# Kernel tuning notes

Measured on AMD Instinct MI355X. Metric: run time of the kernel, lower is better.

Reference implementation:

```python
import jax, jax.numpy as jnp
import numpy as np

NUM_CLASSES = 80
S = 7            # grid_size
NB = 2           # num_boxes per cell
LAMBDA_COORD = 5.0
LAMBDA_NOOBJ = 0.5
N_BOX = 20       # padded boxes per image


def setup_inputs() -> dict:
    key = jax.random.key(0)
    k1, k2, k3, k4 = jax.random.split(key, 4)
    B = 4096
    predictions = jax.random.uniform(k1, (B, S, S, NB, 5 + NUM_CLASSES), dtype=jnp.float32)
    # build valid normalized xyxy boxes: centers in [0.1,0.9], half-sizes in [0.01,0.085]
    centers = jax.random.uniform(k2, (B, N_BOX, 2), dtype=jnp.float32) * 0.8 + 0.1
    half = jax.random.uniform(k3, (B, N_BOX, 2), dtype=jnp.float32) * 0.075 + 0.01
    targets_boxes = jnp.concatenate([centers - half, centers + half], axis=-1)
    targets_labels = jax.random.randint(k4, (B, N_BOX), 0, NUM_CLASSES)
    return {"predictions": predictions, "targets_boxes": targets_boxes, "targets_labels": targets_labels}


def encode_targets(boxes, labels):
    # boxes: [B,N,4] xyxy normalized; labels: [B,N] int
    B, N, _ = boxes.shape
    x = (boxes[..., 0] + boxes[..., 2]) * 0.5
    y = (boxes[..., 1] + boxes[..., 3]) * 0.5
    w = boxes[..., 2] - boxes[..., 0]
    h = boxes[..., 3] - boxes[..., 1]
    j = jnp.clip(jnp.floor(x * S).astype(jnp.int32), 0, S - 1)
    i = jnp.clip(jnp.floor(y * S).astype(jnp.int32), 0, S - 1)
    x_cell = x * S - j
    y_cell = y * S - i
    onehot = jax.nn.one_hot(labels, NUM_CLASSES, dtype=boxes.dtype)
    feats = jnp.concatenate([x_cell[..., None], y_cell[..., None], w[..., None], h[..., None],
                             jnp.ones_like(x_cell)[..., None], onehot], axis=-1)  # [B,N,5+C]
    bidx = jnp.arange(B, dtype=jnp.int32)[:, None]
    flat = ((bidx * S + i) * S + j).ravel()                       # [B*N] cell ids
    order = jnp.broadcast_to(jnp.arange(N, dtype=jnp.int32), (B, N)).ravel()
    winner = jnp.full((B * S * S,), N, dtype=jnp.int32).at[flat].min(order)
    cell_b = jnp.arange(B * S * S, dtype=jnp.int32) // (S * S)
    sel = jnp.minimum(winner, N - 1)
    grid = feats[cell_b, sel]
    grid = jnp.where((winner < N)[:, None], grid, jnp.zeros_like(grid))
    return grid.reshape(B, S, S, 5 + NUM_CLASSES)


def iou_xywh(a, b):
    ax1 = a[..., 0] - a[..., 2] * 0.5; ay1 = a[..., 1] - a[..., 3] * 0.5
    ax2 = a[..., 0] + a[..., 2] * 0.5; ay2 = a[..., 1] + a[..., 3] * 0.5
    bx1 = b[..., 0] - b[..., 2] * 0.5; by1 = b[..., 1] - b[..., 3] * 0.5
    bx2 = b[..., 0] + b[..., 2] * 0.5; by2 = b[..., 1] + b[..., 3] * 0.5
    iw = jnp.clip(jnp.minimum(ax2, bx2) - jnp.maximum(ax1, bx1), 0.0)
    ih = jnp.clip(jnp.minimum(ay2, by2) - jnp.maximum(ay1, by1), 0.0)
    inter = iw * ih
    union = (ax2 - ax1) * (ay2 - ay1) + (bx2 - bx1) * (by2 - by1) - inter
    return inter / (union + 1e-6)


def yolo_loss(predictions, targets_boxes, targets_labels):
    B = predictions.shape[0]
    tg = encode_targets(targets_boxes, targets_labels)   # [B,S,S,5+C]
    txy, twh = tg[..., :2], tg[..., 2:4]
    tconf, tcls = tg[..., 4:5], tg[..., 5:]
    obj = (tconf[..., 0] > 0).astype(predictions.dtype)   # [B,S,S]
    # responsible box = argmax IoU per cell, masked by obj
    pred_boxes = predictions[..., 0:4]                     # [B,S,S,NB,4]
    tgt_boxes = jnp.concatenate([txy, twh], axis=-1)[:, :, :, None, :]
    ious = iou_xywh(pred_boxes, jnp.broadcast_to(tgt_boxes, pred_boxes.shape))  # [B,S,S,NB]
    best = jnp.argmax(ious, axis=-1)
    resp = jax.nn.one_hot(best, NB, dtype=predictions.dtype) * obj[..., None]   # [B,S,S,NB]
    pxy = predictions[..., 0:2]; pwh = predictions[..., 2:4]
    pconf = predictions[..., 4:5]; pcls = predictions[..., 5:]
    om = obj[..., None, None]        # [B,S,S,1,1]
    rm = resp[..., None]             # [B,S,S,NB,1]
    loss_xy = LAMBDA_COORD * jnp.sum(om * rm * (pxy - txy[:, :, :, None, :]) ** 2) / B
    loss_wh = LAMBDA_COORD * jnp.sum(om * rm * (jnp.sqrt(jnp.clip(pwh, 1e-6)) - jnp.sqrt(jnp.clip(twh[:, :, :, None, :], 1e-6))) ** 2) / B
    loss_conf_obj = jnp.sum(om * rm * (pconf - tconf[:, :, :, None, :]) ** 2) / B
    loss_conf_noobj = LAMBDA_NOOBJ * jnp.sum((1.0 - obj)[..., None, None] * pconf ** 2) / B
    pred_cls_resp = jnp.sum(pcls * rm, axis=3)             # [B,S,S,C]
    loss_cls = jnp.sum(obj[..., None] * (pred_cls_resp - tcls) ** 2) / B
    return loss_xy + loss_wh + loss_conf_obj + loss_conf_noobj + loss_cls


def reference(predictions, targets_boxes, targets_labels):
    return yolo_loss(predictions, targets_boxes, targets_labels)
```

## Files before the change

kernel.cpp:

```cpp
#include <hip/hip_runtime.h>

#define S 7
#define NB 2
#define NC 80
#define NBOX 20
#define CELLS 49
#define CH 85
#define PAIR 170
#define PER_B 8330
#define NIMG 4096
#define NCELL_TOT (NIMG*CELLS)
#define N4TOT (NIMG*PER_B/4)
#define PREP_IMGS 4
#define PREP_BLOCKS (NIMG/PREP_IMGS)
#define STREAM_BLOCKS 2048
#define TSTRIDE (STREAM_BLOCKS*256)
#define L_COORD 5.0f
#define L_NOOBJ 0.5f

__device__ __forceinline__ void block_reduce_store(float acc, float* dst)
{
    __shared__ float s_wsum[4];
    int tid = threadIdx.x;
    #pragma unroll
    for (int off = 32; off > 0; off >>= 1) acc += __shfl_down(acc, off, 64);
    int lane = tid & 63, wv = tid >> 6;
    if (lane == 0) s_wsum[wv] = acc;
    __syncthreads();
    if (tid == 0) *dst = s_wsum[0] + s_wsum[1] + s_wsum[2] + s_wsum[3];
}

__global__ __launch_bounds__(256) void prep_kernel(
    const float* __restrict__ pred,
    const float* __restrict__ boxes,
    const int*   __restrict__ labels,
    float4*      __restrict__ wt4,
    float*       __restrict__ partial)
{
    __shared__ int   s_winner[PREP_IMGS * CELLS];
    __shared__ float s_cx[PREP_IMGS * NBOX], s_cy[PREP_IMGS * NBOX];
    __shared__ float s_bw[PREP_IMGS * NBOX], s_bh[PREP_IMGS * NBOX];
    __shared__ int   s_lab[PREP_IMGS * NBOX];

    const int b0  = blockIdx.x * PREP_IMGS;
    const int tid = threadIdx.x;

    if (tid < PREP_IMGS * CELLS) s_winner[tid] = NBOX;
    __syncthreads();

    if (tid < PREP_IMGS * NBOX) {
        int img = tid / NBOX, bxi = tid - img * NBOX;
        const float* bx = boxes + ((size_t)(b0 + img) * NBOX + bxi) * 4;
        float x1 = bx[0], y1 = bx[1], x2 = bx[2], y2 = bx[3];
        float x = (x1 + x2) * 0.5f, y = (y1 + y2) * 0.5f;
        s_cx[tid] = x; s_cy[tid] = y;
        s_bw[tid] = x2 - x1; s_bh[tid] = y2 - y1;
        s_lab[tid] = labels[(size_t)(b0 + img) * NBOX + bxi];
        int j = (int)floorf(x * (float)S); j = min(max(j, 0), S - 1);
        int i = (int)floorf(y * (float)S); i = min(max(i, 0), S - 1);
        atomicMin(&s_winner[img * CELLS + i * S + j], bxi);
    }
    __syncthreads();

    float acc = 0.0f;
    if (tid < PREP_IMGS * CELLS) {
        int img  = tid / CELLS;
        int cell = tid - img * CELLS;
        int w    = s_winner[tid];
        float4 wq;
        if (w < NBOX) {
            int i = cell / S, j = cell - (cell / S) * S;
            int bi = img * NBOX + w;
            float x = s_cx[bi], y = s_cy[bi];
            float tx = x * (float)S - (float)j;
            float ty = y * (float)S - (float)i;
            float tw = s_bw[bi], th = s_bh[bi];

            const float* p = pred + ((size_t)(b0 + img) * CELLS + cell) * PAIR;
            float bx1 = tx - tw * 0.5f, by1 = ty - th * 0.5f;
            float bx2 = tx + tw * 0.5f, by2 = ty + th * 0.5f;
            float barea = (bx2 - bx1) * (by2 - by1);
            float iou[2], px[2], py[2], pw[2], ph[2];
            #pragma unroll
            for (int nb = 0; nb < NB; nb++) {
                px[nb] = p[nb * CH + 0]; py[nb] = p[nb * CH + 1];
                pw[nb] = p[nb * CH + 2]; ph[nb] = p[nb * CH + 3];
                float ax1 = px[nb] - pw[nb] * 0.5f, ay1 = py[nb] - ph[nb] * 0.5f;
                float ax2 = px[nb] + pw[nb] * 0.5f, ay2 = py[nb] + ph[nb] * 0.5f;
                float iw = fmaxf(fminf(ax2, bx2) - fmaxf(ax1, bx1), 0.0f);
                float ih = fmaxf(fminf(ay2, by2) - fmaxf(ay1, by1), 0.0f);
                float inter = iw * ih;
                float uni = (ax2 - ax1) * (ay2 - ay1) + barea - inter;
                iou[nb] = inter / (uni + 1e-6f);
            }
            int resp = (iou[1] > iou[0]) ? 1 : 0;
            wq = (resp == 0) ? make_float4(1.f, 1.f, 0.f, 0.f)
                             : make_float4(0.f, 0.f, 1.f, 1.f);

            float pc = p[resp * CH + 4];
            float pl = p[resp * CH + 5 + s_lab[bi]];
            float dx = px[resp] - tx, dy = py[resp] - ty;
            float dw = sqrtf(fmaxf(pw[resp], 1e-6f)) - sqrtf(fmaxf(tw, 1e-6f));
            float dh = sqrtf(fmaxf(ph[resp], 1e-6f)) - sqrtf(fmaxf(th, 1e-6f));
            acc = L_COORD * (dx * dx + dy * dy + dw * dw + dh * dh)
                + (1.0f - 2.0f * pc)
                + (1.0f - 2.0f * pl);
        } else {
            wq = make_float4(L_NOOBJ, 0.f, L_NOOBJ, 0.f);
        }
        wt4[(size_t)(b0 + img) * CELLS + cell] = wq;
    }
    __syncthreads();
    block_reduce_store(acc, &partial[blockIdx.x]);
}

__device__ __forceinline__ float elem1(float p, int r, float4 w)
{
    int nb = (r >= CH) ? 1 : 0;
    int rr = r - nb * CH;
    float wconf = nb ? w.z : w.x;
    float wcls  = nb ? w.w : w.y;
    float m = (rr >= 5) ? wcls : ((rr == 4) ? wconf : 0.0f);
    return m * p * p;
}

__device__ __forceinline__ float elem4(float4 v, int e,
                                       const float4* __restrict__ wt4)
{
    unsigned ff = 4u * (unsigned)e;
    unsigned c0 = ff / (unsigned)PAIR;
    int r0 = (int)(ff - c0 * (unsigned)PAIR);
    float4 w0 = wt4[c0];
    float4 w1 = w0;
    bool wrap = (r0 == PAIR - 2);
    if (wrap) w1 = wt4[c0 + 1];
    int r2 = wrap ? 0 : r0 + 2;
    float a;
    a  = elem1(v.x, r0,     w0);
    a += elem1(v.y, r0 + 1, w0);
    a += elem1(v.z, r2,     w1);
    a += elem1(v.w, r2 + 1, w1);
    return a;
}

__global__ __launch_bounds__(256) void stream_kernel(
    const float4* __restrict__ p4,
    const float4* __restrict__ wt4,
    float*        __restrict__ partial)
{
    const int tid = threadIdx.x;
    const int gid = blockIdx.x * 256 + tid;

    float acc = 0.0f;
    int e = gid;
    #pragma unroll 8
    for (int k = 0; k < 16; ++k) {
        acc += elem4(p4[e], e, wt4);
        e += TSTRIDE;
    }
    if (e < N4TOT) acc += elem4(p4[e], e, wt4);

    block_reduce_store(acc, &partial[blockIdx.x]);
}

__global__ __launch_bounds__(256) void reduce_kernel(
    const float* __restrict__ partial, int n,
    float* __restrict__ out, float inv_B)
{
    const int tid = threadIdx.x;
    float acc = 0.0f;
    for (int i = tid; i < n; i += 256) acc += partial[i];
    __shared__ float s_wsum[4];
    #pragma unroll
    for (int off = 32; off > 0; off >>= 1) acc += __shfl_down(acc, off, 64);
    int lane = tid & 63, wv = tid >> 6;
    if (lane == 0) s_wsum[wv] = acc;
    __syncthreads();
    if (tid == 0) out[0] = (s_wsum[0] + s_wsum[1] + s_wsum[2] + s_wsum[3]) * inv_B;
}

extern "C" void kernel_launch(void* const* d_in, const int* in_sizes, int n_in,
                              void* d_out, int out_size, void* d_ws, size_t ws_size,
                              hipStream_t stream) {
    const float* pred   = (const float*)d_in[0];
    const float* boxes  = (const float*)d_in[1];
    const int*   labels = (const int*)d_in[2];

    float4* wt4          = (float4*)d_ws;
    float*  prep_part    = (float*)d_ws + (size_t)NCELL_TOT * 4;
    float*  stream_part  = prep_part + PREP_BLOCKS;

    prep_kernel<<<PREP_BLOCKS, 256, 0, stream>>>(pred, boxes, labels, wt4, prep_part);
    stream_kernel<<<STREAM_BLOCKS, 256, 0, stream>>>((const float4*)pred, wt4, stream_part);
    reduce_kernel<<<1, 256, 0, stream>>>(prep_part, PREP_BLOCKS + STREAM_BLOCKS,
                                         (float*)d_out, 1.0f / (float)NIMG);
}
```

Measured before the change: 203.3 us.

## Fuse target prep and prediction streaming into one per-image-pair kernel

Merges the prep and stream kernels so each block handles two images. It builds the per-cell weight table in shared memory and then streams that pair's predictions against it. This removes the global weight-table write and read-back and one kernel launch, and reads box coordinates as float4. The cost is 2048 blocks doing a serial prep phase before streaming, with reads that are contiguous per block rather than grid-strided, plus the cold per-cell prediction loads now on the critical path.

```diff
diff --git a/kernel.cpp b/kernel.cpp
--- a/kernel.cpp
+++ b/kernel.cpp
@@ -9,12 +9,10 @@
 #define PAIR 170
 #define PER_B 8330
 #define NIMG 4096
-#define NCELL_TOT (NIMG*CELLS)
-#define N4TOT (NIMG*PER_B/4)
-#define PREP_IMGS 4
-#define PREP_BLOCKS (NIMG/PREP_IMGS)
-#define STREAM_BLOCKS 2048
-#define TSTRIDE (STREAM_BLOCKS*256)
+#define IMGS_PER_BLK 2
+#define NPAIR (NIMG/IMGS_PER_BLK)
+#define F4_PER_PAIR (PER_B*IMGS_PER_BLK/4)
+#define CELLS2 (CELLS*IMGS_PER_BLK)
 #define L_COORD 5.0f
 #define L_NOOBJ 0.5f
 
@@ -30,32 +28,60 @@
     if (tid == 0) *dst = s_wsum[0] + s_wsum[1] + s_wsum[2] + s_wsum[3];
 }
 
-__global__ __launch_bounds__(256) void prep_kernel(
-    const float* __restrict__ pred,
-    const float* __restrict__ boxes,
-    const int*   __restrict__ labels,
-    float4*      __restrict__ wt4,
-    float*       __restrict__ partial)
+__device__ __forceinline__ float elem1(float p, int r, float4 w)
 {
-    __shared__ int   s_winner[PREP_IMGS * CELLS];
-    __shared__ float s_cx[PREP_IMGS * NBOX], s_cy[PREP_IMGS * NBOX];
-    __shared__ float s_bw[PREP_IMGS * NBOX], s_bh[PREP_IMGS * NBOX];
-    __shared__ int   s_lab[PREP_IMGS * NBOX];
+    int nb = (r >= CH) ? 1 : 0;
+    int rr = r - nb * CH;
+    float wconf = nb ? w.z : w.x;
+    float wcls  = nb ? w.w : w.y;
+    float m = (rr >= 5) ? wcls : ((rr == 4) ? wconf : 0.0f);
+    return m * p * p;
+}
 
-    const int b0  = blockIdx.x * PREP_IMGS;
+__device__ __forceinline__ float elem4(float4 v, int e, const float4* s_wq)
+{
+    unsigned ff = 4u * (unsigned)e;
+    unsigned c0 = ff / (unsigned)PAIR;
+    int r0 = (int)(ff - c0 * (unsigned)PAIR);
+    float4 w0 = s_wq[c0];
+    float4 w1 = w0;
+    bool wrap = (r0 == PAIR - 2);
+    if (wrap) w1 = s_wq[c0 + 1];
+    int r2 = wrap ? 0 : r0 + 2;
+    float a;
+    a  = elem1(v.x, r0,     w0);
+    a += elem1(v.y, r0 + 1, w0);
+    a += elem1(v.z, r2,     w1);
+    a += elem1(v.w, r2 + 1, w1);
+    return a;
+}
+
+__global__ __launch_bounds__(256) void fused_kernel(
+    const float4* __restrict__ p4,
+    const float4* __restrict__ boxes4,
+    const int*    __restrict__ labels,
+    float*        __restrict__ partial)
+{
+    __shared__ int    s_winner[CELLS2];
+    __shared__ float  s_cx[IMGS_PER_BLK * NBOX], s_cy[IMGS_PER_BLK * NBOX];
+    __shared__ float  s_bw[IMGS_PER_BLK * NBOX], s_bh[IMGS_PER_BLK * NBOX];
+    __shared__ int    s_lab[IMGS_PER_BLK * NBOX];
+    __shared__ float4 s_wq[CELLS2];
+
+    const int pb  = blockIdx.x;
     const int tid = threadIdx.x;
 
-    if (tid < PREP_IMGS * CELLS) s_winner[tid] = NBOX;
+    if (tid < CELLS2) s_winner[tid] = NBOX;
     __syncthreads();
 
-    if (tid < PREP_IMGS * NBOX) {
+    if (tid < IMGS_PER_BLK * NBOX) {
         int img = tid / NBOX, bxi = tid - img * NBOX;
-        const float* bx = boxes + ((size_t)(b0 + img) * NBOX + bxi) * 4;
-        float x1 = bx[0], y1 = bx[1], x2 = bx[2], y2 = bx[3];
-        float x = (x1 + x2) * 0.5f, y = (y1 + y2) * 0.5f;
+        size_t gbox = (size_t)(pb * IMGS_PER_BLK + img) * NBOX + bxi;
+        float4 bx = boxes4[gbox];
+        float x = (bx.x + bx.z) * 0.5f, y = (bx.y + bx.w) * 0.5f;
         s_cx[tid] = x; s_cy[tid] = y;
-        s_bw[tid] = x2 - x1; s_bh[tid] = y2 - y1;
-        s_lab[tid] = labels[(size_t)(b0 + img) * NBOX + bxi];
+        s_bw[tid] = bx.z - bx.x; s_bh[tid] = bx.w - bx.y;
+        s_lab[tid] = labels[gbox];
         int j = (int)floorf(x * (float)S); j = min(max(j, 0), S - 1);
         int i = (int)floorf(y * (float)S); i = min(max(i, 0), S - 1);
         atomicMin(&s_winner[img * CELLS + i * S + j], bxi);
@@ -63,7 +89,7 @@
     __syncthreads();
 
     float acc = 0.0f;
-    if (tid < PREP_IMGS * CELLS) {
+    if (tid < CELLS2) {
         int img  = tid / CELLS;
         int cell = tid - img * CELLS;
         int w    = s_winner[tid];
@@ -76,7 +102,9 @@
             float ty = y * (float)S - (float)i;
             float tw = s_bw[bi], th = s_bh[bi];
 
-            const float* p = pred + ((size_t)(b0 + img) * CELLS + cell) * PAIR;
+            const float* p = (const float*)p4
+                           + (size_t)(pb * IMGS_PER_BLK + img) * PER_B
+                           + (size_t)cell * PAIR;
             float bx1 = tx - tw * 0.5f, by1 = ty - th * 0.5f;
             float bx2 = tx + tw * 0.5f, by2 = ty + th * 0.5f;
             float barea = (bx2 - bx1) * (by2 - by1);
@@ -108,59 +136,22 @@
         } else {
             wq = make_float4(L_NOOBJ, 0.f, L_NOOBJ, 0.f);
         }
-        wt4[(size_t)(b0 + img) * CELLS + cell] = wq;
+        s_wq[tid] = wq;
     }
     __syncthreads();
-    block_reduce_store(acc, &partial[blockIdx.x]);
-}
 
-__device__ __forceinline__ float elem1(float p, int r, float4 w)
-{
-    int nb = (r >= CH) ? 1 : 0;
-    int rr = r - nb * CH;
-    float wconf = nb ? w.z : w.x;
-    float wcls  = nb ? w.w : w.y;
-    float m = (rr >= 5) ? wcls : ((rr == 4) ? wconf : 0.0f);
-    return m * p * p;
-}
+    const float4* p = p4 + (size_t)pb * F4_PER_PAIR;
+    #pragma unroll
+    for (int k = 0; k < 16; ++k) {
+        int e = tid + (k << 8);
+        acc += elem4(p[e], e, s_wq);
+    }
+    {
+        int e = tid + 4096;
+        if (tid < F4_PER_PAIR - 4096) acc += elem4(p[e], e, s_wq);
+    }
 
-__device__ __forceinline__ float elem4(float4 v, int e,
-                                       const float4* __restrict__ wt4)
-{
-    unsigned ff = 4u * (unsigned)e;
-    unsigned c0 = ff / (unsigned)PAIR;
-    int r0 = (int)(ff - c0 * (unsigned)PAIR);
-    float4 w0 = wt4[c0];
-    float4 w1 = w0;
-    bool wrap = (r0 == PAIR - 2);
-    if (wrap) w1 = wt4[c0 + 1];
-    int r2 = wrap ? 0 : r0 + 2;
-    float a;
-    a  = elem1(v.x, r0,     w0);
-    a += elem1(v.y, r0 + 1, w0);
-    a += elem1(v.z, r2,     w1);
-    a += elem1(v.w, r2 + 1, w1);
-    return a;
-}
-
-__global__ __launch_bounds__(256) void stream_kernel(
-    const float4* __restrict__ p4,
-    const float4* __restrict__ wt4,
-    float*        __restrict__ partial)
-{
-    const int tid = threadIdx.x;
-    const int gid = blockIdx.x * 256 + tid;
-
-    float acc = 0.0f;
-    int e = gid;
-    #pragma unroll 8
-    for (int k = 0; k < 16; ++k) {
-        acc += elem4(p4[e], e, wt4);
-        e += TSTRIDE;
-    }
-    if (e < N4TOT) acc += elem4(p4[e], e, wt4);
-
-    block_reduce_store(acc, &partial[blockIdx.x]);
+    block_reduce_store(acc, &partial[pb]);
 }
 
 __global__ __launch_bounds__(256) void reduce_kernel(
@@ -186,12 +177,10 @@
     const float* boxes  = (const float*)d_in[1];
     const int*   labels = (const int*)d_in[2];
 
-    float4* wt4          = (float4*)d_ws;
-    float*  prep_part    = (float*)d_ws + (size_t)NCELL_TOT * 4;
-    float*  stream_part  = prep_part + PREP_BLOCKS;
+    float* partial = (float*)d_ws;
 
-    prep_kernel<<<PREP_BLOCKS, 256, 0, stream>>>(pred, boxes, labels, wt4, prep_part);
-    stream_kernel<<<STREAM_BLOCKS, 256, 0, stream>>>((const float4*)pred, wt4, stream_part);
-    reduce_kernel<<<1, 256, 0, stream>>>(prep_part, PREP_BLOCKS + STREAM_BLOCKS,
+    fused_kernel<<<NPAIR, 256, 0, stream>>>((const float4*)pred,
+                                            (const float4*)boxes, labels, partial);
+    reduce_kernel<<<1, 256, 0, stream>>>(partial, NPAIR,
                                          (float*)d_out, 1.0f / (float)NIMG);
 }
```

Measured after the change: 201.9 us. No clear change (-0.7%).
